# Optimization experiments

Measured on AMD Instinct MI355X. Metric: run time of the kernel, lower is better.

## Reference

```python
import jax, jax.numpy as jnp
import numpy as np

HIDDEN_DIM = 640
VOCAB_SIZE = 1024


def setup_inputs() -> dict:
    key = jax.random.key(0)
    kf, kp, kw, kb = jax.random.split(key, 4)
    B, T, U, H, V = 8, 256, 64, HIDDEN_DIM, VOCAB_SIZE
    f = jax.random.normal(kf, (B, T, H), dtype=jnp.float32)
    p = jax.random.normal(kp, (B, U, H), dtype=jnp.float32)
    # nn.Linear default init: U(-1/sqrt(H), 1/sqrt(H))
    bound = 1.0 / np.sqrt(H)
    W = jax.random.uniform(kw, (V, H), minval=-bound, maxval=bound, dtype=jnp.float32)
    b = jax.random.uniform(kb, (V,), minval=-bound, maxval=bound, dtype=jnp.float32)
    return {"f": f, "p": p, "W": W, "b": b}


def reference(f, p, W, b):
    # f: (B,T,H), p: (B,U,H) -> combined: (B,T,U,H)
    combined = f[:, :, None, :] + p[:, None, :, :]
    h = jax.nn.relu(combined)
    # Linear: h @ W^T + b -> (B,T,U,V)
    logits = jnp.einsum('btuh,vh->btuv', h, W) + b
    return logits
```

## Files before the change

kernel.cpp:

```cpp
#include <hip/hip_runtime.h>
#include <hip/hip_bf16.h>

#define BDIM 8
#define TDIM 256
#define UDIM 64
#define HDIM 640
#define VDIM 1024
#define MDIM (BDIM * TDIM * UDIM)

#define BM 128
#define BN 128
#define BK 32
#define NT (HDIM / BK)
#define NBUF 3

typedef __attribute__((ext_vector_type(8))) short short8;
typedef __attribute__((ext_vector_type(4))) float f32x4;

__device__ __forceinline__ ushort f2bf(float x) {
    union { float f; unsigned int u; } v; v.f = x;
    unsigned int r = (v.u + 0x7fffu + ((v.u >> 16) & 1u)) >> 16;
    return (ushort)r;
}

__global__ void cvt_w_kernel(const float* __restrict__ W, ushort* __restrict__ Wb) {
    int i = (blockIdx.x * 256 + threadIdx.x) * 4;
    f32x4 w = *(const f32x4*)(W + i);
    ushort4 o;
    o.x = f2bf(w[0]); o.y = f2bf(w[1]); o.z = f2bf(w[2]); o.w = f2bf(w[3]);
    *(ushort4*)(Wb + i) = o;
}

__global__ __launch_bounds__(256) void build_h_kernel(
    const float* __restrict__ f, const float* __restrict__ p,
    ushort* __restrict__ h)
{
    const int tid = threadIdx.x;
    const int row = (blockIdx.x << 5) + (tid >> 3);
    const int j0  = tid & 7;
    const int b = row >> 14;
    const int t = (row >> 6) & (TDIM - 1);
    const int u = row & (UDIM - 1);
    const float* frow = f + (size_t)(b * TDIM + t) * HDIM;
    const float* prow = p + (size_t)(b * UDIM + u) * HDIM;
    ushort* hrow = h + (size_t)row * HDIM;
    #pragma unroll
    for (int it = 0; it < HDIM / 64; ++it) {
        const int k = (j0 + it * 8) * 8;
        f32x4 f0 = *(const f32x4*)(frow + k);
        f32x4 f1 = *(const f32x4*)(frow + k + 4);
        f32x4 p0 = *(const f32x4*)(prow + k);
        f32x4 p1 = *(const f32x4*)(prow + k + 4);
        short8 hv;
        #pragma unroll
        for (int e = 0; e < 4; ++e) {
            float a0 = fmaxf(f0[e] + p0[e], 0.0f);
            float a1 = fmaxf(f1[e] + p1[e], 0.0f);
            hv[e]     = (short)f2bf(a0);
            hv[e + 4] = (short)f2bf(a1);
        }
        *(short8*)(hrow + k) = hv;
    }
}

#define GLDS(srcptr, ldsptr)                                                   \
    __builtin_amdgcn_global_load_lds(                                          \
        (const __attribute__((address_space(1))) void*)(srcptr),               \
        (__attribute__((address_space(3))) void*)(ldsptr), 16, 0, 0)

__global__ __launch_bounds__(256, 3) void hgemm128_kernel(
    const ushort* __restrict__ h,
    const ushort* __restrict__ Wb,
    const float* __restrict__ bias,
    float* __restrict__ out)
{
    __shared__ ushort Ash[NBUF][BM * BK];
    __shared__ ushort Bsh[NBUF][BN * BK];

    const int tid  = threadIdx.x;
    const int lane = tid & 63;
    const int wave = tid >> 6;
    const int wm   = wave >> 1;
    const int wn   = wave & 1;

    const int bid   = blockIdx.x;
    const int work  = (bid & 7) * 1024 + (bid >> 3);
    const int mtile = work >> 3;
    const int ntile = work & 7;
    const int m0 = mtile * BM;
    const int v0 = ntile * BN;

    const ushort* hbase = h  + (size_t)m0 * HDIM;
    const ushort* wbase = Wb + (size_t)v0 * HDIM;

    const int r0a = tid >> 2;
    const int r0b = r0a + 64;
    const int j0  = tid & 3;
    const size_t sof0 = (size_t)r0a * HDIM + (j0 ^ ((r0a >> 1) & 3)) * 8;
    const size_t sof1 = (size_t)r0b * HDIM + (j0 ^ ((r0b >> 1) & 3)) * 8;
    const int u0 = (wave * 64) * 8;
    const int u1 = (256 + wave * 64) * 8;

    int aoff[4], boff[4];
    #pragma unroll
    for (int mi = 0; mi < 4; ++mi) {
        const int r = wm * 64 + mi * 16 + (lane & 15);
        aoff[mi] = (r * 4 + ((lane >> 4) ^ ((r >> 1) & 3))) * 8;
    }
    #pragma unroll
    for (int ni = 0; ni < 4; ++ni) {
        const int r = wn * 64 + ni * 16 + (lane & 15);
        boff[ni] = (r * 4 + ((lane >> 4) ^ ((r >> 1) & 3))) * 8;
    }

    f32x4 acc[4][4];
    #pragma unroll
    for (int i = 0; i < 4; ++i)
        #pragma unroll
        for (int j = 0; j < 4; ++j)
            acc[i][j] = (f32x4)0.0f;

#define STG(kt, bf) do {                                                       \
        GLDS(hbase + sof0 + (kt) * BK, &Ash[bf][u0]);                          \
        GLDS(hbase + sof1 + (kt) * BK, &Ash[bf][u1]);                          \
        GLDS(wbase + sof0 + (kt) * BK, &Bsh[bf][u0]);                          \
        GLDS(wbase + sof1 + (kt) * BK, &Bsh[bf][u1]);                          \
    } while (0)

    STG(0, 0);
    STG(1, 1);

    int d = 0;
    int e = 2;
    #pragma unroll 1
    for (int t = 0; t < NT; ++t) {
        if (t < NT - 1) { asm volatile("s_waitcnt vmcnt(4)" ::: "memory"); }
        else            { asm volatile("s_waitcnt vmcnt(0)" ::: "memory"); }
        __builtin_amdgcn_sched_barrier(0);
        __builtin_amdgcn_s_barrier();
        __builtin_amdgcn_sched_barrier(0);

        short8 afr[4], bfr[4];
        #pragma unroll
        for (int q = 0; q < 4; ++q) {
            afr[q] = *(const short8*)(&Ash[d][aoff[q]]);
            bfr[q] = *(const short8*)(&Bsh[d][boff[q]]);
        }

        if (t + 2 < NT) STG(t + 2, e);

        __builtin_amdgcn_s_setprio(1);
        #pragma unroll
        for (int mi = 0; mi < 4; ++mi)
            #pragma unroll
            for (int ni = 0; ni < 4; ++ni)
                acc[mi][ni] = __builtin_amdgcn_mfma_f32_16x16x32_bf16(
                    afr[mi], bfr[ni], acc[mi][ni], 0, 0, 0);
        __builtin_amdgcn_s_setprio(0);
        __builtin_amdgcn_sched_barrier(0);

        d = (d == NBUF - 1) ? 0 : d + 1;
        e = (e == NBUF - 1) ? 0 : e + 1;
    }
#undef STG

    #pragma unroll
    for (int ni = 0; ni < 4; ++ni) {
        const int col = v0 + wn * 64 + ni * 16 + (lane & 15);
        const float bv = bias[col];
        #pragma unroll
        for (int mi = 0; mi < 4; ++mi) {
            const int rbase = m0 + wm * 64 + mi * 16 + ((lane >> 4) << 2);
            #pragma unroll
            for (int reg = 0; reg < 4; ++reg) {
                out[(size_t)(rbase + reg) * VDIM + col] = acc[mi][ni][reg] + bv;
            }
        }
    }
}

template <bool USE_WB>
__global__ __launch_bounds__(256) void joint_gemm_kernel(
    const float* __restrict__ f, const float* __restrict__ p,
    const float* __restrict__ Wf, const ushort* __restrict__ Wb,
    const float* __restrict__ bias, float* __restrict__ out)
{
    __shared__ ushort Alds[128 * 64];
    __shared__ ushort Blds[128 * 64];

    const int tid  = threadIdx.x;
    const int lane = tid & 63;
    const int wave = tid >> 6;
    const int wm   = wave >> 1;
    const int wn   = wave & 1;

    const int bid   = blockIdx.x;
    const int work  = (bid & 7) * 1024 + (bid >> 3);
    const int mtile = work >> 3;
    const int ntile = work & 7;
    const int m0 = mtile * 128;
    const int v0 = ntile * 128;

    const int b  = m0 >> 14;
    const int t0 = (m0 >> 6) & (TDIM - 1);

    const float*  fbase = f + (size_t)(b * TDIM + t0) * HDIM;
    const float*  pbase = p + (size_t)b * UDIM * HDIM;
    const ushort* wbbase = Wb + (size_t)v0 * HDIM;
    const float*  wfbase = Wf + (size_t)v0 * HDIM;

    f32x4 acc[4][4];
    #pragma unroll
    for (int i = 0; i < 4; ++i)
        #pragma unroll
        for (int j = 0; j < 4; ++j)
            acc[i][j] = (f32x4)0.0f;

    for (int kt = 0; kt < HDIM / 64; ++kt) {
        const int k0 = kt * 64;
        __syncthreads();

        if (USE_WB) {
            #pragma unroll
            for (int it = 0; it < 4; ++it) {
                const int c   = it * 256 + tid;
                const int row = c >> 3;
                const int j   = c & 7;
                const ushort* src = wbbase + row * HDIM + k0 + ((j ^ (row & 7)) << 3);
                GLDS(src, &Blds[(it * 256 + wave * 64) * 8]);
            }
        } else {
            #pragma unroll
            for (int it = 0; it < 4; ++it) {
                const int c   = it * 256 + tid;
                const int row = c >> 3;
                const int j   = c & 7;
                const float* wp = wfbase + row * HDIM + k0 + j * 8;
                f32x4 w0 = *(const f32x4*)wp;
                f32x4 w1 = *(const f32x4*)(wp + 4);
                short8 wv;
                #pragma unroll
                for (int e = 0; e < 4; ++e) {
                    wv[e]     = (short)f2bf(w0[e]);
                    wv[e + 4] = (short)f2bf(w1[e]);
                }
                *(short8*)(&Blds[(row * 8 + (j ^ (row & 7))) * 8]) = wv;
            }
        }

        #pragma unroll
        for (int it = 0; it < 4; ++it) {
            const int c   = it * 256 + tid;
            const int row = c >> 3;
            const int j   = c & 7;
            const float* fp_ = fbase + (row >> 6) * HDIM + k0 + j * 8;
            const float* pp_ = pbase + (row & 63) * HDIM + k0 + j * 8;
            f32x4 f0 = *(const f32x4*)fp_;
            f32x4 f1 = *(const f32x4*)(fp_ + 4);
            f32x4 p0 = *(const f32x4*)pp_;
            f32x4 p1 = *(const f32x4*)(pp_ + 4);
            short8 hv;
            #pragma unroll
            for (int e = 0; e < 4; ++e) {
                float a0 = fmaxf(f0[e] + p0[e], 0.0f);
                float a1 = fmaxf(f1[e] + p1[e], 0.0f);
                hv[e]     = (short)f2bf(a0);
                hv[e + 4] = (short)f2bf(a1);
            }
            *(short8*)(&Alds[(row * 8 + (j ^ (row & 7))) * 8]) = hv;
        }

        __syncthreads();

        #pragma unroll
        for (int ks = 0; ks < 2; ++ks) {
            short8 afr[4], bfr[4];
            #pragma unroll
            for (int mi = 0; mi < 4; ++mi) {
                const int r = wm * 64 + mi * 16 + (lane & 15);
                const int j = ks * 4 + (lane >> 4);
                afr[mi] = *(const short8*)(&Alds[(r * 8 + (j ^ (r & 7))) * 8]);
            }
            #pragma unroll
            for (int ni = 0; ni < 4; ++ni) {
                const int r = wn * 64 + ni * 16 + (lane & 15);
                const int j = ks * 4 + (lane >> 4);
                bfr[ni] = *(const short8*)(&Blds[(r * 8 + (j ^ (r & 7))) * 8]);
            }
            #pragma unroll
            for (int mi = 0; mi < 4; ++mi)
                #pragma unroll
                for (int ni = 0; ni < 4; ++ni)
                    acc[mi][ni] = __builtin_amdgcn_mfma_f32_16x16x32_bf16(
                        afr[mi], bfr[ni], acc[mi][ni], 0, 0, 0);
        }
    }

    #pragma unroll
    for (int ni = 0; ni < 4; ++ni) {
        const int col = v0 + wn * 64 + ni * 16 + (lane & 15);
        const float bv = bias[col];
        #pragma unroll
        for (int mi = 0; mi < 4; ++mi) {
            const int rbase = m0 + wm * 64 + mi * 16 + ((lane >> 4) << 2);
            #pragma unroll
            for (int reg = 0; reg < 4; ++reg) {
                out[(size_t)(rbase + reg) * VDIM + col] = acc[mi][ni][reg] + bv;
            }
        }
    }
}

extern "C" void kernel_launch(void* const* d_in, const int* in_sizes, int n_in,
                              void* d_out, int out_size, void* d_ws, size_t ws_size,
                              hipStream_t stream) {
    const float* f    = (const float*)d_in[0];
    const float* p    = (const float*)d_in[1];
    const float* W    = (const float*)d_in[2];
    const float* bias = (const float*)d_in[3];
    float* out = (float*)d_out;

    const size_t wb_bytes = (size_t)VDIM * HDIM * sizeof(ushort);
    const size_t h_bytes  = (size_t)MDIM * HDIM * sizeof(ushort);

    if (ws_size >= wb_bytes + h_bytes) {
        ushort* Wb = (ushort*)d_ws;
        ushort* h  = (ushort*)((char*)d_ws + wb_bytes);
        cvt_w_kernel<<<(VDIM * HDIM) / 1024, 256, 0, stream>>>(W, Wb);
        build_h_kernel<<<MDIM / 32, 256, 0, stream>>>(f, p, h);
        const int grid = (MDIM / BM) * (VDIM / BN);
        hgemm128_kernel<<<grid, 256, 0, stream>>>(h, Wb, bias, out);
    } else if (ws_size >= wb_bytes) {
        ushort* Wb = (ushort*)d_ws;
        cvt_w_kernel<<<(VDIM * HDIM) / 1024, 256, 0, stream>>>(W, Wb);
        joint_gemm_kernel<true><<<(MDIM / 128) * (VDIM / 128), 256, 0, stream>>>(
            f, p, W, Wb, bias, out);
    } else {
        joint_gemm_kernel<false><<<(MDIM / 128) * (VDIM / 128), 256, 0, stream>>>(
            f, p, W, nullptr, bias, out);
    }
}
```

Baseline: 376.4 us.

## Fuse relu(f+p) bf16 construction into GEMM A-tile staging, drop h buffer

Removes the separate build_h pass and its bf16 intermediate matrix, which is about 42 MB written and then read back. Each GEMM block now loads f and p in fp32 from global memory, computes relu and converts to bf16 in registers, and writes the A tile to LDS. The B tile still arrives through async global_load_lds. The pipeline goes from three LDS buffers to two with an extra barrier per k-step, and the launch bound is raised to 4 blocks per SM. In exchange, f and p are re-read by all 8 column-tile blocks, the conversion math is repeated for each of them, and less load latency is hidden because every step waits on vmcnt(0).

```diff
diff --git a/kernel.cpp b/kernel.cpp
--- a/kernel.cpp
+++ b/kernel.cpp
@@ -8,11 +8,8 @@
 #define VDIM 1024
 #define MDIM (BDIM * TDIM * UDIM)
 
-#define BM 128
-#define BN 128
 #define BK 32
 #define NT (HDIM / BK)
-#define NBUF 3
 
 typedef __attribute__((ext_vector_type(8))) short short8;
 typedef __attribute__((ext_vector_type(4))) float f32x4;
@@ -31,51 +28,20 @@
     *(ushort4*)(Wb + i) = o;
 }
 
-__global__ __launch_bounds__(256) void build_h_kernel(
-    const float* __restrict__ f, const float* __restrict__ p,
-    ushort* __restrict__ h)
-{
-    const int tid = threadIdx.x;
-    const int row = (blockIdx.x << 5) + (tid >> 3);
-    const int j0  = tid & 7;
-    const int b = row >> 14;
-    const int t = (row >> 6) & (TDIM - 1);
-    const int u = row & (UDIM - 1);
-    const float* frow = f + (size_t)(b * TDIM + t) * HDIM;
-    const float* prow = p + (size_t)(b * UDIM + u) * HDIM;
-    ushort* hrow = h + (size_t)row * HDIM;
-    #pragma unroll
-    for (int it = 0; it < HDIM / 64; ++it) {
-        const int k = (j0 + it * 8) * 8;
-        f32x4 f0 = *(const f32x4*)(frow + k);
-        f32x4 f1 = *(const f32x4*)(frow + k + 4);
-        f32x4 p0 = *(const f32x4*)(prow + k);
-        f32x4 p1 = *(const f32x4*)(prow + k + 4);
-        short8 hv;
-        #pragma unroll
-        for (int e = 0; e < 4; ++e) {
-            float a0 = fmaxf(f0[e] + p0[e], 0.0f);
-            float a1 = fmaxf(f1[e] + p1[e], 0.0f);
-            hv[e]     = (short)f2bf(a0);
-            hv[e + 4] = (short)f2bf(a1);
-        }
-        *(short8*)(hrow + k) = hv;
-    }
-}
-
 #define GLDS(srcptr, ldsptr)                                                   \
     __builtin_amdgcn_global_load_lds(                                          \
         (const __attribute__((address_space(1))) void*)(srcptr),               \
         (__attribute__((address_space(3))) void*)(ldsptr), 16, 0, 0)
 
-__global__ __launch_bounds__(256, 3) void hgemm128_kernel(
-    const ushort* __restrict__ h,
+__global__ __launch_bounds__(256, 4) void fused128_kernel(
+    const float* __restrict__ f,
+    const float* __restrict__ p,
     const ushort* __restrict__ Wb,
     const float* __restrict__ bias,
     float* __restrict__ out)
 {
-    __shared__ ushort Ash[NBUF][BM * BK];
-    __shared__ ushort Bsh[NBUF][BN * BK];
+    __shared__ ushort Ash[2][128 * BK];
+    __shared__ ushort Bsh[2][128 * BK];
 
     const int tid  = threadIdx.x;
     const int lane = tid & 63;
@@ -87,19 +53,33 @@
     const int work  = (bid & 7) * 1024 + (bid >> 3);
     const int mtile = work >> 3;
     const int ntile = work & 7;
-    const int m0 = mtile * BM;
-    const int v0 = ntile * BN;
-
-    const ushort* hbase = h  + (size_t)m0 * HDIM;
+    const int m0 = mtile * 128;
+    const int v0 = ntile * 128;
+
     const ushort* wbase = Wb + (size_t)v0 * HDIM;
 
     const int r0a = tid >> 2;
     const int r0b = r0a + 64;
     const int j0  = tid & 3;
-    const size_t sof0 = (size_t)r0a * HDIM + (j0 ^ ((r0a >> 1) & 3)) * 8;
-    const size_t sof1 = (size_t)r0b * HDIM + (j0 ^ ((r0b >> 1) & 3)) * 8;
+    const size_t sofB0 = (size_t)r0a * HDIM + (j0 ^ ((r0a >> 1) & 3)) * 8;
+    const size_t sofB1 = (size_t)r0b * HDIM + (j0 ^ ((r0b >> 1) & 3)) * 8;
     const int u0 = (wave * 64) * 8;
     const int u1 = (256 + wave * 64) * 8;
+
+    int foffc[2], poffc[2], dstc[2];
+    #pragma unroll
+    for (int i = 0; i < 2; ++i) {
+        const int c   = i * 256 + tid;
+        const int row = c >> 2;
+        const int j   = c & 3;
+        const int m   = m0 + row;
+        const int b   = m >> 14;
+        const int t   = (m >> 6) & (TDIM - 1);
+        const int u   = m & (UDIM - 1);
+        foffc[i] = (b * TDIM + t) * HDIM + j * 8;
+        poffc[i] = (b * UDIM + u) * HDIM + j * 8;
+        dstc[i]  = (row * 4 + (j ^ ((row >> 1) & 3))) * 8;
+    }
 
     int aoff[4], boff[4];
     #pragma unroll
@@ -120,22 +100,41 @@
         for (int j = 0; j < 4; ++j)
             acc[i][j] = (f32x4)0.0f;
 
-#define STG(kt, bf) do {                                                       \
-        GLDS(hbase + sof0 + (kt) * BK, &Ash[bf][u0]);                          \
-        GLDS(hbase + sof1 + (kt) * BK, &Ash[bf][u1]);                          \
-        GLDS(wbase + sof0 + (kt) * BK, &Bsh[bf][u0]);                          \
-        GLDS(wbase + sof1 + (kt) * BK, &Bsh[bf][u1]);                          \
+#define CONSTRUCT_A(kk, bf) do {                                               \
+        _Pragma("unroll")                                                      \
+        for (int i_ = 0; i_ < 2; ++i_) {                                       \
+            const float* fp_ = f + foffc[i_] + (kk);                           \
+            const float* pp_ = p + poffc[i_] + (kk);                           \
+            f32x4 f0_ = *(const f32x4*)fp_;                                    \
+            f32x4 f1_ = *(const f32x4*)(fp_ + 4);                              \
+            f32x4 p0_ = *(const f32x4*)pp_;                                    \
+            f32x4 p1_ = *(const f32x4*)(pp_ + 4);                              \
+            short8 hv_;                                                        \
+            _Pragma("unroll")                                                  \
+            for (int e_ = 0; e_ < 4; ++e_) {                                   \
+                float a0_ = fmaxf(f0_[e_] + p0_[e_], 0.0f);                    \
+                float a1_ = fmaxf(f1_[e_] + p1_[e_], 0.0f);                    \
+                hv_[e_]     = (short)f2bf(a0_);                                \
+                hv_[e_ + 4] = (short)f2bf(a1_);                                \
+            }                                                                  \
+            *(short8*)(&Ash[bf][dstc[i_]]) = hv_;                              \
+        }                                                                      \
     } while (0)
 
-    STG(0, 0);
-    STG(1, 1);
+#define STG_B(kk, bf) do {                                                     \
+        GLDS(wbase + sofB0 + (kk), &Bsh[bf][u0]);                              \
+        GLDS(wbase + sofB1 + (kk), &Bsh[bf][u1]);                              \
+    } while (0)
+
+    CONSTRUCT_A(0, 0);
+    STG_B(0, 0);
+    asm volatile("s_waitcnt lgkmcnt(0)" ::: "memory");
 
     int d = 0;
-    int e = 2;
     #pragma unroll 1
     for (int t = 0; t < NT; ++t) {
-        if (t < NT - 1) { asm volatile("s_waitcnt vmcnt(4)" ::: "memory"); }
-        else            { asm volatile("s_waitcnt vmcnt(0)" ::: "memory"); }
+        const int e = d ^ 1;
+        asm volatile("s_waitcnt vmcnt(0)" ::: "memory");
         __builtin_amdgcn_sched_barrier(0);
         __builtin_amdgcn_s_barrier();
         __builtin_amdgcn_sched_barrier(0);
@@ -147,7 +146,11 @@
             bfr[q] = *(const short8*)(&Bsh[d][boff[q]]);
         }
 
-        if (t + 2 < NT) STG(t + 2, e);
+        if (t + 1 < NT) {
+            const int kk = (t + 1) * BK;
+            CONSTRUCT_A(kk, e);
+            STG_B(kk, e);
+        }
 
         __builtin_amdgcn_s_setprio(1);
         #pragma unroll
@@ -157,12 +160,14 @@
                 acc[mi][ni] = __builtin_amdgcn_mfma_f32_16x16x32_bf16(
                     afr[mi], bfr[ni], acc[mi][ni], 0, 0, 0);
         __builtin_amdgcn_s_setprio(0);
+
+        asm volatile("s_waitcnt lgkmcnt(0)" ::: "memory");
         __builtin_amdgcn_sched_barrier(0);
-
-        d = (d == NBUF - 1) ? 0 : d + 1;
-        e = (e == NBUF - 1) ? 0 : e + 1;
-    }
-#undef STG
+        __builtin_amdgcn_s_barrier();
+        d = e;
+    }
+#undef STG_B
+#undef CONSTRUCT_A
 
     #pragma unroll
     for (int ni = 0; ni < 4; ++ni) {
@@ -321,22 +326,14 @@
     float* out = (float*)d_out;
 
     const size_t wb_bytes = (size_t)VDIM * HDIM * sizeof(ushort);
-    const size_t h_bytes  = (size_t)MDIM * HDIM * sizeof(ushort);
-
-    if (ws_size >= wb_bytes + h_bytes) {
-        ushort* Wb = (ushort*)d_ws;
-        ushort* h  = (ushort*)((char*)d_ws + wb_bytes);
-        cvt_w_kernel<<<(VDIM * HDIM) / 1024, 256, 0, stream>>>(W, Wb);
-        build_h_kernel<<<MDIM / 32, 256, 0, stream>>>(f, p, h);
-        const int grid = (MDIM / BM) * (VDIM / BN);
-        hgemm128_kernel<<<grid, 256, 0, stream>>>(h, Wb, bias, out);
-    } else if (ws_size >= wb_bytes) {
+    const int grid = (MDIM / 128) * (VDIM / 128);
+
+    if (ws_size >= wb_bytes) {
         ushort* Wb = (ushort*)d_ws;
         cvt_w_kernel<<<(VDIM * HDIM) / 1024, 256, 0, stream>>>(W, Wb);
-        joint_gemm_kernel<true><<<(MDIM / 128) * (VDIM / 128), 256, 0, stream>>>(
-            f, p, W, Wb, bias, out);
+        fused128_kernel<<<grid, 256, 0, stream>>>(f, p, Wb, bias, out);
     } else {
-        joint_gemm_kernel<false><<<(MDIM / 128) * (VDIM / 128), 256, 0, stream>>>(
+        joint_gemm_kernel<false><<<grid, 256, 0, stream>>>(
             f, p, W, nullptr, bias, out);
     }
 }
```

After: 377.7 us. About the same (+0.4%).
